# Optimization experiments

Measured on AMD Instinct MI355X. Metric: run time of the kernel, lower is better.

Reference implementation:

```python
import jax, jax.numpy as jnp
import numpy as np

C = 256
RATE_CHOICE = [32, 64, 96, 128, 160, 192, 224, 256]
RATE_NUM = len(RATE_CHOICE)
MAX_RATE = max(RATE_CHOICE)
B, H, W = 16, 16, 16


def setup_inputs() -> dict:
    key = jax.random.key(0)
    k_x, k_idx, k_w = jax.random.split(key, 3)
    x = jax.random.normal(k_x, (B, C, H, W), dtype=jnp.float32)
    indexes = jax.random.randint(k_idx, (B * H * W,), 0, RATE_NUM, dtype=jnp.int64)
    # xavier_normal over (fan_in=C*MAX_RATE? torch 3D: fan_in=C*MAX_RATE, fan_out=RATE_NUM*MAX_RATE) -> use gain std
    std = float(np.sqrt(2.0 / (C + MAX_RATE)))
    weight = jax.random.normal(k_w, (RATE_NUM, C, MAX_RATE), dtype=jnp.float32) * std
    bias = jnp.zeros((RATE_NUM, MAX_RATE), dtype=jnp.float32)
    rate_choice_tensor = jnp.asarray(RATE_CHOICE, dtype=jnp.int32)
    return {"x": x, "indexes": indexes, "weight": weight, "bias": bias,
            "rate_choice_tensor": rate_choice_tensor}


def reference(x, indexes, weight, bias, rate_choice_tensor):
    Bv, Cv, Hv, Wv = x.shape
    L = Hv * Wv
    R = weight.shape[-1]
    # x: [B,C,H,W] -> [B,L,C]
    x_blc = x.reshape(Bv, Cv, L).transpose(0, 2, 1)
    # per-token gathered weights/bias
    w = weight[indexes].reshape(Bv, L, Cv, R)      # [B,L,C,R]
    b = bias[indexes].reshape(Bv, L, R)            # [B,L,R]
    # rate mask: arange(R) < rate_choice[idx]
    rc = rate_choice_tensor[indexes].reshape(Bv, L, 1)
    mask = (jnp.arange(R, dtype=rc.dtype)[None, None, :] < rc).astype(x.dtype)  # [B,L,R]
    # batched per-token matvec + bias, then mask
    y = (jnp.einsum('blc,blcr->blr', x_blc, w) + b) * mask
    x_masked = y.reshape(Bv, Hv, Wv, R).transpose(0, 3, 1, 2)     # [B,R,H,W]
    mask_bchw = mask.reshape(Bv, Hv, Wv, R).transpose(0, 3, 1, 2)
    return (x_masked, mask_bchw)
```

## Files before the change

### kernel.cpp

```cpp
#include <hip/hip_runtime.h>

#define WS_CNT    0
#define WS_BUCKET 8192
#define WS_WT     (1 << 20)
#define WS_XT     (2 << 20)
#define WS_YT     (6 << 20)
#define WS_NEED   (10 << 20)

typedef short v8s __attribute__((ext_vector_type(8)));
typedef float v4f __attribute__((ext_vector_type(4)));

__device__ __forceinline__ unsigned short bf16_rne(float f) {
  unsigned int u = __float_as_uint(f);
  return (unsigned short)((u + 0x7fffu + ((u >> 16) & 1u)) >> 16);
}
__device__ __forceinline__ float bf16_to_f(unsigned short h) {
  return __uint_as_float(((unsigned int)h) << 16);
}

__global__ __launch_bounds__(256) void prep_kernel(const float* __restrict__ x,
                                                   const int* __restrict__ idx,
                                                   const float* __restrict__ W,
                                                   int* __restrict__ cnt,
                                                   int* __restrict__ bucket2,
                                                   short* __restrict__ Wt,
                                                   float* __restrict__ xT) {
  const int bid = blockIdx.x;
  const int tid = threadIdx.x;

  if (bid < 256) {
    __shared__ float tile[32][33];
    for (int k = 0; k < 4; ++k) {
      const int tau = (bid << 2) + k;
      const int b = tau >> 6;
      const int c0 = ((tau & 63) >> 3) << 5;
      const int l0 = (tau & 7) << 5;
      const int j = tid & 31;
      const int i = tid >> 5;
      if (k) __syncthreads();
#pragma unroll
      for (int ii = 0; ii < 4; ++ii)
        tile[(ii << 3) + i][j] = x[(b << 16) + ((c0 + (ii << 3) + i) << 8) + l0 + j];
      __syncthreads();
#pragma unroll
      for (int ii = 0; ii < 4; ++ii)
        xT[(((b << 8) + l0 + (ii << 3) + i) << 8) + c0 + j] = tile[j][(ii << 3) + i];
    }
  } else if (bid < 512) {
    __shared__ short ts[32][33];
    for (int k2 = 0; k2 < 2; ++k2) {
      const int tau = ((bid - 256) << 1) + k2;
      const int gg = tau >> 6;
      const int ti = tau & 63;
      const int c0 = (ti >> 3) << 5;
      const int r0 = (ti & 7) << 5;
      const int j = tid & 31, i = tid >> 5;
      if (k2) __syncthreads();
#pragma unroll
      for (int ii = 0; ii < 4; ++ii) {
        const int ci = (ii << 3) + i;
        ts[ci][j] = (short)bf16_rne(W[(gg << 16) + ((c0 + ci) << 8) + r0 + j]);
      }
      __syncthreads();
      const int p = tid & 15, q = tid >> 4;
#pragma unroll
      for (int rr = 0; rr < 2; ++rr) {
        const int rj = (rr << 4) + q;
        const unsigned int val =
            (unsigned int)(unsigned short)ts[(p << 1)][rj] |
            ((unsigned int)(unsigned short)ts[(p << 1) + 1][rj] << 16);
        *(unsigned int*)(Wt + (gg << 16) + ((r0 + rj) << 8) + c0 + (p << 1)) = val;
      }
    }
  } else {
    __shared__ int lcount[8];
    const int b = bid - 512;
    if (tid < 8) lcount[tid] = 0;
    __syncthreads();
    const int t = (b << 8) + tid;
    const int g = idx[t];
    const int p = atomicAdd(&lcount[g], 1);
    bucket2[(((b << 3) + g) << 8) + p] = t;
    __syncthreads();
    if (tid < 8) cnt[(b << 3) + tid] = lcount[tid];
  }
}

__global__ __launch_bounds__(256) void gemm_kernel(const float* __restrict__ xT,
                                                   const short* __restrict__ Wt,
                                                   const float* __restrict__ bias,
                                                   const int* __restrict__ cnt,
                                                   const int* __restrict__ bucket2,
                                                   float* __restrict__ yT) {
  const int g = blockIdx.x;
  const int tid = threadIdx.x;

  __shared__ int scnt[16];
  __shared__ int toks[32];
  __shared__ __align__(16) short As[2][32][264];

  if (tid < 16) scnt[tid] = cnt[(tid << 3) + g];
  __syncthreads();
  int n = 0;
#pragma unroll
  for (int b2 = 0; b2 < 16; ++b2) n += scnt[b2];
  const int t0 = blockIdx.y << 5;
  if (t0 >= n) return;
  const int ntv = min(32, n - t0);

  if (tid < 32) {
    const int sl = min(t0 + tid, n - 1);
    int acc = 0, bsel = 0, off = 0;
#pragma unroll
    for (int b2 = 0; b2 < 16; ++b2) {
      const int c2 = scnt[b2];
      if (sl >= acc && sl < acc + c2) { bsel = b2; off = sl - acc; }
      acc += c2;
    }
    toks[tid] = bucket2[(((bsel << 3) + g) << 8) + off];
  }
  __syncthreads();

  {
    const int tk = tid >> 3, sub = tid & 7;
    const float* src = xT + (toks[tk] << 8) + (sub << 2);
#pragma unroll
    for (int q = 0; q < 8; ++q) {
      const float4 v = *reinterpret_cast<const float4*>(src + (q << 5));
      const int c = (sub << 2) + (q << 5);
      const unsigned short h0 = bf16_rne(v.x), h1 = bf16_rne(v.y);
      const unsigned short h2 = bf16_rne(v.z), h3 = bf16_rne(v.w);
      const unsigned short e0 = bf16_rne(v.x - bf16_to_f(h0));
      const unsigned short e1 = bf16_rne(v.y - bf16_to_f(h1));
      const unsigned short e2 = bf16_rne(v.z - bf16_to_f(h2));
      const unsigned short e3 = bf16_rne(v.w - bf16_to_f(h3));
      uint2 ph, pl;
      ph.x = (unsigned int)h0 | ((unsigned int)h1 << 16);
      ph.y = (unsigned int)h2 | ((unsigned int)h3 << 16);
      pl.x = (unsigned int)e0 | ((unsigned int)e1 << 16);
      pl.y = (unsigned int)e2 | ((unsigned int)e3 << 16);
      *reinterpret_cast<uint2*>(&As[0][tk][c]) = ph;
      *reinterpret_cast<uint2*>(&As[1][tk][c]) = pl;
    }
  }
  __syncthreads();

  const int lane = tid & 63, wid = tid >> 6;
  const int mt = wid & 1;
  const int nr = (wid >> 1) << 7;
  const int li = lane & 15, quad = lane >> 4;
  const short* Bg = Wt + (g << 16);

  v4f acc[8];
#pragma unroll
  for (int nt = 0; nt < 8; ++nt) acc[nt] = (v4f){0.f, 0.f, 0.f, 0.f};

  v8s b0[8], b1[8];
#pragma unroll
  for (int nt = 0; nt < 8; ++nt)
    b0[nt] = *reinterpret_cast<const v8s*>(Bg + ((nr + (nt << 4) + li) << 8) + (quad << 3));

#pragma unroll
  for (int ks = 0; ks < 8; ++ks) {
    const v8s ah = *reinterpret_cast<const v8s*>(&As[0][(mt << 4) + li][(ks << 5) + (quad << 3)]);
    const v8s al = *reinterpret_cast<const v8s*>(&As[1][(mt << 4) + li][(ks << 5) + (quad << 3)]);
    v8s* bc = (ks & 1) ? b1 : b0;
    v8s* bn = (ks & 1) ? b0 : b1;
    if (ks < 7) {
#pragma unroll
      for (int nt = 0; nt < 8; ++nt)
        bn[nt] = *reinterpret_cast<const v8s*>(
            Bg + ((nr + (nt << 4) + li) << 8) + ((ks + 1) << 5) + (quad << 3));
    }
#pragma unroll
    for (int nt = 0; nt < 8; ++nt) {
      acc[nt] = __builtin_amdgcn_mfma_f32_16x16x32_bf16(ah, bc[nt], acc[nt], 0, 0, 0);
      acc[nt] = __builtin_amdgcn_mfma_f32_16x16x32_bf16(al, bc[nt], acc[nt], 0, 0, 0);
    }
  }

  int tok4[4]; bool ok4[4];
#pragma unroll
  for (int reg = 0; reg < 4; ++reg) {
    const int m = (mt << 4) + (quad << 2) + reg;
    ok4[reg] = (m < ntv);
    tok4[reg] = toks[m];
  }
#pragma unroll
  for (int nt = 0; nt < 8; ++nt) {
    const int nn = nr + (nt << 4) + li;
    const float bv = bias[(g << 8) + nn];
#pragma unroll
    for (int reg = 0; reg < 4; ++reg) {
      if (ok4[reg]) yT[(tok4[reg] << 8) + nn] = acc[nt][reg] + bv;
    }
  }
}

__global__ __launch_bounds__(256) void out_kernel(const float* __restrict__ yT,
                                                  const int* __restrict__ idx,
                                                  const int* __restrict__ rate,
                                                  float* __restrict__ out) {
  __shared__ float tile[32][33];
  __shared__ int rcl[32];
  const int b = blockIdx.x;
  const int r0 = (blockIdx.y >> 3) << 5;
  const int l0 = (blockIdx.y & 7) << 5;
  const int j = threadIdx.x & 31;
  const int i = threadIdx.x >> 5;
#pragma unroll
  for (int ii = 0; ii < 4; ++ii) {
    const int l = l0 + (ii << 3) + i;
    tile[(ii << 3) + i][j] = yT[(((b << 8) + l) << 8) + r0 + j];
  }
  if (threadIdx.x < 32) rcl[threadIdx.x] = rate[idx[(b << 8) + l0 + threadIdx.x]];
  __syncthreads();
#pragma unroll
  for (int ii = 0; ii < 4; ++ii) {
    const int r = r0 + (ii << 3) + i;
    const float m = (r < rcl[j]) ? 1.0f : 0.0f;
    const int o = (b << 16) + (r << 8) + l0 + j;
    out[o] = tile[j][(ii << 3) + i] * m;
    out[(1 << 20) + o] = m;
  }
}

__global__ __launch_bounds__(256) void rate_tok_kernel(
    const float* __restrict__ x, const int* __restrict__ indexes,
    const float* __restrict__ W, const float* __restrict__ bias,
    const int* __restrict__ rate, float* __restrict__ out) {
  const int t = blockIdx.x;
  const int b = t >> 8;
  const int l = t & 255;
  const int r = threadIdx.x;
  __shared__ float xs[256];
  xs[r] = x[(b << 16) + (r << 8) + l];
  const int g = indexes[t];
  const int rc = rate[g];
  __syncthreads();
  const float* w = W + (g << 16) + r;
  float acc = bias[(g << 8) + r];
#pragma unroll 8
  for (int c = 0; c < 256; ++c) acc += xs[c] * w[c << 8];
  const float m = (r < rc) ? 1.0f : 0.0f;
  const int o = (b << 16) + (r << 8) + l;
  out[o] = acc * m;
  out[(1 << 20) + o] = m;
}

extern "C" void kernel_launch(void* const* d_in, const int* in_sizes, int n_in,
                              void* d_out, int out_size, void* d_ws, size_t ws_size,
                              hipStream_t stream) {
  const float* x    = (const float*)d_in[0];
  const int*   idx  = (const int*)d_in[1];
  const float* W    = (const float*)d_in[2];
  const float* bias = (const float*)d_in[3];
  const int*   rate = (const int*)d_in[4];
  float* out = (float*)d_out;
  char*  ws  = (char*)d_ws;

  if (ws_size >= (size_t)WS_NEED) {
    int*   cnt     = (int*)(ws + WS_CNT);
    int*   bucket2 = (int*)(ws + WS_BUCKET);
    short* Wt      = (short*)(ws + WS_WT);
    float* xT      = (float*)(ws + WS_XT);
    float* yT      = (float*)(ws + WS_YT);
    prep_kernel<<<dim3(528), dim3(256), 0, stream>>>(x, idx, W, cnt, bucket2, Wt, xT);
    gemm_kernel<<<dim3(8, 24), dim3(256), 0, stream>>>(xT, Wt, bias, cnt, bucket2, yT);
    out_kernel<<<dim3(16, 64), dim3(256), 0, stream>>>(yT, idx, rate, out);
  } else {
    rate_tok_kernel<<<dim3(4096), dim3(256), 0, stream>>>(x, idx, W, bias, rate, out);
  }
}
```

Baseline: 88.32 us.

## Split prep into one tile per block and halve GEMM token tile

The prep kernel now gives each block a single transpose tile instead of looping over four or two, which triples the grid to 1552 blocks. The gemm kernel processes 16 tokens per block instead of 32, doubling the grid to 8x48, and each wave now covers 64 output columns. Bias is folded into the accumulator init and counts are read straight from global memory. The aim is more parallelism on a small problem, at the cost of each Wt tile being reloaded by twice as many blocks.

```diff
diff --git a/kernel.cpp b/kernel.cpp
--- a/kernel.cpp
+++ b/kernel.cpp
@@ -28,53 +28,46 @@
   const int bid = blockIdx.x;
   const int tid = threadIdx.x;
 
-  if (bid < 256) {
+  if (bid < 1024) {
     __shared__ float tile[32][33];
-    for (int k = 0; k < 4; ++k) {
-      const int tau = (bid << 2) + k;
-      const int b = tau >> 6;
-      const int c0 = ((tau & 63) >> 3) << 5;
-      const int l0 = (tau & 7) << 5;
-      const int j = tid & 31;
-      const int i = tid >> 5;
-      if (k) __syncthreads();
-#pragma unroll
-      for (int ii = 0; ii < 4; ++ii)
-        tile[(ii << 3) + i][j] = x[(b << 16) + ((c0 + (ii << 3) + i) << 8) + l0 + j];
-      __syncthreads();
-#pragma unroll
-      for (int ii = 0; ii < 4; ++ii)
-        xT[(((b << 8) + l0 + (ii << 3) + i) << 8) + c0 + j] = tile[j][(ii << 3) + i];
-    }
-  } else if (bid < 512) {
+    const int b = bid >> 6;
+    const int c0 = ((bid & 63) >> 3) << 5;
+    const int l0 = (bid & 7) << 5;
+    const int j = tid & 31;
+    const int i = tid >> 5;
+#pragma unroll
+    for (int ii = 0; ii < 4; ++ii)
+      tile[(ii << 3) + i][j] = x[(b << 16) + ((c0 + (ii << 3) + i) << 8) + l0 + j];
+    __syncthreads();
+#pragma unroll
+    for (int ii = 0; ii < 4; ++ii)
+      xT[(((b << 8) + l0 + (ii << 3) + i) << 8) + c0 + j] = tile[j][(ii << 3) + i];
+  } else if (bid < 1536) {
     __shared__ short ts[32][33];
-    for (int k2 = 0; k2 < 2; ++k2) {
-      const int tau = ((bid - 256) << 1) + k2;
-      const int gg = tau >> 6;
-      const int ti = tau & 63;
-      const int c0 = (ti >> 3) << 5;
-      const int r0 = (ti & 7) << 5;
-      const int j = tid & 31, i = tid >> 5;
-      if (k2) __syncthreads();
-#pragma unroll
-      for (int ii = 0; ii < 4; ++ii) {
-        const int ci = (ii << 3) + i;
-        ts[ci][j] = (short)bf16_rne(W[(gg << 16) + ((c0 + ci) << 8) + r0 + j]);
-      }
-      __syncthreads();
-      const int p = tid & 15, q = tid >> 4;
-#pragma unroll
-      for (int rr = 0; rr < 2; ++rr) {
-        const int rj = (rr << 4) + q;
-        const unsigned int val =
-            (unsigned int)(unsigned short)ts[(p << 1)][rj] |
-            ((unsigned int)(unsigned short)ts[(p << 1) + 1][rj] << 16);
-        *(unsigned int*)(Wt + (gg << 16) + ((r0 + rj) << 8) + c0 + (p << 1)) = val;
-      }
+    const int tau = bid - 1024;
+    const int gg = tau >> 6;
+    const int ti = tau & 63;
+    const int c0 = (ti >> 3) << 5;
+    const int r0 = (ti & 7) << 5;
+    const int j = tid & 31, i = tid >> 5;
+#pragma unroll
+    for (int ii = 0; ii < 4; ++ii) {
+      const int ci = (ii << 3) + i;
+      ts[ci][j] = (short)bf16_rne(W[(gg << 16) + ((c0 + ci) << 8) + r0 + j]);
+    }
+    __syncthreads();
+    const int p = tid & 15, q = tid >> 4;
+#pragma unroll
+    for (int rr = 0; rr < 2; ++rr) {
+      const int rj = (rr << 4) + q;
+      const unsigned int val =
+          (unsigned int)(unsigned short)ts[(p << 1)][rj] |
+          ((unsigned int)(unsigned short)ts[(p << 1) + 1][rj] << 16);
+      *(unsigned int*)(Wt + (gg << 16) + ((r0 + rj) << 8) + c0 + (p << 1)) = val;
     }
   } else {
     __shared__ int lcount[8];
-    const int b = bid - 512;
+    const int b = bid - 1536;
     if (tid < 8) lcount[tid] = 0;
     __syncthreads();
     const int t = (b << 8) + tid;
@@ -95,25 +88,22 @@
   const int g = blockIdx.x;
   const int tid = threadIdx.x;
 
-  __shared__ int scnt[16];
-  __shared__ int toks[32];
-  __shared__ __align__(16) short As[2][32][264];
-
-  if (tid < 16) scnt[tid] = cnt[(tid << 3) + g];
-  __syncthreads();
   int n = 0;
 #pragma unroll
-  for (int b2 = 0; b2 < 16; ++b2) n += scnt[b2];
-  const int t0 = blockIdx.y << 5;
+  for (int b2 = 0; b2 < 16; ++b2) n += cnt[(b2 << 3) + g];
+  const int t0 = blockIdx.y << 4;
   if (t0 >= n) return;
-  const int ntv = min(32, n - t0);
-
-  if (tid < 32) {
+  const int ntv = min(16, n - t0);
+
+  __shared__ int toks[16];
+  __shared__ __align__(16) short As[2][16][264];
+
+  if (tid < 16) {
     const int sl = min(t0 + tid, n - 1);
     int acc = 0, bsel = 0, off = 0;
 #pragma unroll
     for (int b2 = 0; b2 < 16; ++b2) {
-      const int c2 = scnt[b2];
+      const int c2 = cnt[(b2 << 3) + g];
       if (sl >= acc && sl < acc + c2) { bsel = b2; off = sl - acc; }
       acc += c2;
     }
@@ -122,12 +112,12 @@
   __syncthreads();
 
   {
-    const int tk = tid >> 3, sub = tid & 7;
+    const int tk = tid >> 4, sub = tid & 15;
     const float* src = xT + (toks[tk] << 8) + (sub << 2);
 #pragma unroll
-    for (int q = 0; q < 8; ++q) {
-      const float4 v = *reinterpret_cast<const float4*>(src + (q << 5));
-      const int c = (sub << 2) + (q << 5);
+    for (int q = 0; q < 4; ++q) {
+      const float4 v = *reinterpret_cast<const float4*>(src + (q << 6));
+      const int c = (sub << 2) + (q << 6);
       const unsigned short h0 = bf16_rne(v.x), h1 = bf16_rne(v.y);
       const unsigned short h2 = bf16_rne(v.z), h3 = bf16_rne(v.w);
       const unsigned short e0 = bf16_rne(v.x - bf16_to_f(h0));
@@ -146,53 +136,48 @@
   __syncthreads();
 
   const int lane = tid & 63, wid = tid >> 6;
-  const int mt = wid & 1;
-  const int nr = (wid >> 1) << 7;
+  const int nr = wid << 6;
   const int li = lane & 15, quad = lane >> 4;
   const short* Bg = Wt + (g << 16);
 
-  v4f acc[8];
-#pragma unroll
-  for (int nt = 0; nt < 8; ++nt) acc[nt] = (v4f){0.f, 0.f, 0.f, 0.f};
-
-  v8s b0[8], b1[8];
-#pragma unroll
-  for (int nt = 0; nt < 8; ++nt)
-    b0[nt] = *reinterpret_cast<const v8s*>(Bg + ((nr + (nt << 4) + li) << 8) + (quad << 3));
+  v4f acc[4];
+#pragma unroll
+  for (int nt = 0; nt < 4; ++nt) {
+    const float bv = bias[(g << 8) + nr + (nt << 4) + li];
+    acc[nt] = (v4f){bv, bv, bv, bv};
+  }
+
+  v8s bfr[2][4];
+#pragma unroll
+  for (int nt = 0; nt < 4; ++nt)
+    bfr[0][nt] = *reinterpret_cast<const v8s*>(Bg + ((nr + (nt << 4) + li) << 8) + (quad << 3));
 
 #pragma unroll
   for (int ks = 0; ks < 8; ++ks) {
-    const v8s ah = *reinterpret_cast<const v8s*>(&As[0][(mt << 4) + li][(ks << 5) + (quad << 3)]);
-    const v8s al = *reinterpret_cast<const v8s*>(&As[1][(mt << 4) + li][(ks << 5) + (quad << 3)]);
-    v8s* bc = (ks & 1) ? b1 : b0;
-    v8s* bn = (ks & 1) ? b0 : b1;
+    const v8s ah = *reinterpret_cast<const v8s*>(&As[0][li][(ks << 5) + (quad << 3)]);
+    const v8s al = *reinterpret_cast<const v8s*>(&As[1][li][(ks << 5) + (quad << 3)]);
+    v8s* bc = bfr[ks & 1];
+    v8s* bn = bfr[(ks & 1) ^ 1];
     if (ks < 7) {
 #pragma unroll
-      for (int nt = 0; nt < 8; ++nt)
+      for (int nt = 0; nt < 4; ++nt)
         bn[nt] = *reinterpret_cast<const v8s*>(
             Bg + ((nr + (nt << 4) + li) << 8) + ((ks + 1) << 5) + (quad << 3));
     }
 #pragma unroll
-    for (int nt = 0; nt < 8; ++nt) {
+    for (int nt = 0; nt < 4; ++nt) {
       acc[nt] = __builtin_amdgcn_mfma_f32_16x16x32_bf16(ah, bc[nt], acc[nt], 0, 0, 0);
       acc[nt] = __builtin_amdgcn_mfma_f32_16x16x32_bf16(al, bc[nt], acc[nt], 0, 0, 0);
     }
   }
 
-  int tok4[4]; bool ok4[4];
-#pragma unroll
-  for (int reg = 0; reg < 4; ++reg) {
-    const int m = (mt << 4) + (quad << 2) + reg;
-    ok4[reg] = (m < ntv);
-    tok4[reg] = toks[m];
-  }
-#pragma unroll
-  for (int nt = 0; nt < 8; ++nt) {
+#pragma unroll
+  for (int nt = 0; nt < 4; ++nt) {
     const int nn = nr + (nt << 4) + li;
-    const float bv = bias[(g << 8) + nn];
 #pragma unroll
     for (int reg = 0; reg < 4; ++reg) {
-      if (ok4[reg]) yT[(tok4[reg] << 8) + nn] = acc[nt][reg] + bv;
+      const int m = (quad << 2) + reg;
+      if (m < ntv) yT[(toks[m] << 8) + nn] = acc[nt][reg];
     }
   }
 }
@@ -265,8 +250,8 @@
     short* Wt      = (short*)(ws + WS_WT);
     float* xT      = (float*)(ws + WS_XT);
     float* yT      = (float*)(ws + WS_YT);
-    prep_kernel<<<dim3(528), dim3(256), 0, stream>>>(x, idx, W, cnt, bucket2, Wt, xT);
-    gemm_kernel<<<dim3(8, 24), dim3(256), 0, stream>>>(xT, Wt, bias, cnt, bucket2, yT);
+    prep_kernel<<<dim3(1552), dim3(256), 0, stream>>>(x, idx, W, cnt, bucket2, Wt, xT);
+    gemm_kernel<<<dim3(8, 48), dim3(256), 0, stream>>>(xT, Wt, bias, cnt, bucket2, yT);
     out_kernel<<<dim3(16, 64), dim3(256), 0, stream>>>(yT, idx, rate, out);
   } else {
     rate_tok_kernel<<<dim3(4096), dim3(256), 0, stream>>>(x, idx, W, bias, rate, out);
```

After: 82.85 us. 6.2% less time.
